# Optimization experiments

Measured on AMD Instinct MI355X. Metric: run time of the kernel, lower is better.

## Reference

```python
import jax, jax.numpy as jnp
import numpy as np

N, E = 10000, 160000
B, F, P, C = 16, 2, 12, 32


def gcn_norm(edge_index, edge_weight, n):
    # GCN symmetric normalization with self-loops (fill value 1.0, improved=False)
    src, dst = edge_index[0], edge_index[1]
    loop = jnp.arange(n, dtype=src.dtype)
    src = jnp.concatenate([src, loop])
    dst = jnp.concatenate([dst, loop])
    w = jnp.concatenate([edge_weight, jnp.ones((n,), edge_weight.dtype)])
    deg = jnp.zeros((n,), w.dtype).at[dst].add(w)
    dinv = jnp.where(deg > 0, jax.lax.rsqrt(deg), 0.0)
    return src, dst, dinv[src] * w * dinv[dst]


def gcn_conv(x, W, b, src, dst, norm, n):
    # x: [B, N, Fin] -> [B, N, Fout]; transform-then-propagate like GCNConv
    xw = x @ W
    msgs = xw[:, src, :] * norm[None, :, None]  # gather over source nodes
    out = jnp.zeros((x.shape[0], n, W.shape[1]), x.dtype).at[:, dst].add(msgs)
    return out + b


def setup_inputs():
    key = jax.random.key(0)
    ks = jax.random.split(key, 20)
    s = 0.1
    return {
        "x": jax.random.normal(ks[0], (B, N, F, P), jnp.float32),
        "edge_index": jax.random.randint(ks[1], (2, E), 0, N, jnp.int32),
        "edge_weight": jax.random.uniform(ks[2], (E,), jnp.float32),
        "W_z": jax.random.normal(ks[3], (F, C), jnp.float32) * s,
        "b_z": jnp.zeros((C,), jnp.float32),
        "lin_z_W": jax.random.normal(ks[4], (2 * C, C), jnp.float32) * s,
        "lin_z_b": jnp.zeros((C,), jnp.float32),
        "W_r": jax.random.normal(ks[5], (F, C), jnp.float32) * s,
        "b_r": jnp.zeros((C,), jnp.float32),
        "lin_r_W": jax.random.normal(ks[6], (2 * C, C), jnp.float32) * s,
        "lin_r_b": jnp.zeros((C,), jnp.float32),
        "W_h": jax.random.normal(ks[7], (F, C), jnp.float32) * s,
        "b_h": jnp.zeros((C,), jnp.float32),
        "lin_h_W": jax.random.normal(ks[8], (2 * C, C), jnp.float32) * s,
        "lin_h_b": jnp.zeros((C,), jnp.float32),
        "attention": jax.random.uniform(ks[9], (P,), jnp.float32),
        "lin_out_W": jax.random.normal(ks[10], (C, P), jnp.float32) * s,
        "lin_out_b": jnp.zeros((P,), jnp.float32),
    }


def reference(x, edge_index, edge_weight, W_z, b_z, lin_z_W, lin_z_b, W_r, b_r,
              lin_r_W, lin_r_b, W_h, b_h, lin_h_W, lin_h_b, attention,
              lin_out_W, lin_out_b):
    b, n, f, p = x.shape
    c = W_z.shape[1]
    src, dst, norm = gcn_norm(edge_index, edge_weight, n)
    probs = jax.nn.softmax(attention)  # attention over periods
    H0 = jnp.zeros((b, n, c), x.dtype)  # A3TGCN2 passes H=None each period
    xs = jnp.moveaxis(x, 3, 0)  # [P, B, N, F]

    def step(acc, inp):
        xp, w = inp  # xp: [B, N, F]
        Gz = gcn_conv(xp, W_z, b_z, src, dst, norm, n)
        Z = jax.nn.sigmoid(jnp.concatenate([Gz, H0], -1) @ lin_z_W + lin_z_b)
        Gr = gcn_conv(xp, W_r, b_r, src, dst, norm, n)
        R = jax.nn.sigmoid(jnp.concatenate([Gr, H0], -1) @ lin_r_W + lin_r_b)
        Gh = gcn_conv(xp, W_h, b_h, src, dst, norm, n)
        Ht = jnp.tanh(jnp.concatenate([Gh, H0 * R], -1) @ lin_h_W + lin_h_b)
        Hn = Z * H0 + (1.0 - Z) * Ht  # one GRU step from zero hidden
        return acc + w * Hn, None

    H_acc, _ = jax.lax.scan(step, H0, (xs, probs))
    h = jax.nn.relu(H_acc)
    return h @ lin_out_W + lin_out_b  # [B, N, periods]
```

## Files before the change

### kernel.cpp

```cpp
#include <hip/hip_runtime.h>
#include <hip/hip_bf16.h>

#define NN 10000
#define EE 160000
#define BB 16
#define PP 12
#define CC 32
#define CAP 64
#define NCB 313
#define NHB 625

__device__ __forceinline__ float fast_rcp(float x){ return __builtin_amdgcn_rcpf(x); }
__device__ __forceinline__ float fast_exp2(float x){
#if __has_builtin(__builtin_amdgcn_exp2f)
    return __builtin_amdgcn_exp2f(x);
#else
    return exp2f(x);
#endif
}
__device__ __forceinline__ unsigned short f2bfu(float f){
    union { float f; unsigned int i; } c; c.f = f;
    unsigned int r = c.i + 0x7FFFu + ((c.i >> 16) & 1u);
    return (unsigned short)(r >> 16);
}
__device__ __forceinline__ void up2(unsigned int u, float& a, float& b){
    union { unsigned int i; float f; } c;
    c.i = u << 16;          a = c.f;
    c.i = u & 0xFFFF0000u;  b = c.f;
}
__device__ __forceinline__ void unp24(uint4 q0, uint4 q1, uint4 q2, float* f){
    up2(q0.x,f[0],f[1]);   up2(q0.y,f[2],f[3]);   up2(q0.z,f[4],f[5]);   up2(q0.w,f[6],f[7]);
    up2(q1.x,f[8],f[9]);   up2(q1.y,f[10],f[11]); up2(q1.z,f[12],f[13]); up2(q1.w,f[14],f[15]);
    up2(q2.x,f[16],f[17]); up2(q2.y,f[18],f[19]); up2(q2.z,f[20],f[21]); up2(q2.w,f[22],f[23]);
}

__global__ __launch_bounds__(256) void k_stage(const float* __restrict__ x,
        const int* __restrict__ srcI, const int* __restrict__ dstI,
        const float* __restrict__ ew,
        unsigned short* __restrict__ xc, float* __restrict__ deg, int* __restrict__ cnt,
        int2* __restrict__ bucket, const int* __restrict__ canary_p,
        const float* __restrict__ Wz, const float* __restrict__ bz,
        const float* __restrict__ LzW, const float* __restrict__ lzb,
        const float* __restrict__ Wh, const float* __restrict__ bh,
        const float* __restrict__ LhW, const float* __restrict__ lhb,
        const float* __restrict__ att, const float* __restrict__ LoW,
        const float* __restrict__ lob, float* __restrict__ wbuf){
    __shared__ unsigned short tile[32*384];
    int bid = blockIdx.x, tid = threadIdx.x;
    if (bid < NCB){
        int n0 = bid*32;
        int n1 = NN - n0; if (n1 > 32) n1 = 32;
        int tot = 16 * n1 * 6;
        for (int i = tid; i < tot; i += 256){
            int b = i / (n1*6);
            int r = i - b*(n1*6);
            float4 f = *(const float4*)(x + b*(NN*24) + n0*24 + r*4);
            ushort4 v; v.x=f2bfu(f.x); v.y=f2bfu(f.y); v.z=f2bfu(f.z); v.w=f2bfu(f.w);
            int nl = (r*4) / 24;
            int fp = (r*4) - nl*24;
            ((ushort4*)tile)[nl*96 + (b*24 + fp)/4] = v;
        }
        __syncthreads();
        int tot4 = n1*48;
        uint4* dst4 = (uint4*)(xc + n0*384);
        for (int i = tid; i < tot4; i += 256)
            dst4[i] = ((const uint4*)tile)[i];
    } else if (bid < NCB + NHB){
        int canary = *canary_p;
        int e = (bid - NCB)*256 + tid;
        int d = dstI[e];
        float w = ew[e];
        atomicAdd(&deg[d], w);
        int rk = atomicAdd(&cnt[d], 1) - canary;
        bucket[d*CAP + rk] = make_int2(srcI[e], __float_as_int(w));
    } else {
        const float L2E = 1.4426950408889634f;
        int c = tid;
        if (c < CC){
            float s0=0.f,s1=0.f,sb=lzb[c], h0=0.f,h1=0.f,hb=lhb[c];
            for (int k=0;k<CC;k++){
                float wz = LzW[k*CC+c];
                s0 += Wz[k]*wz; s1 += Wz[CC+k]*wz; sb += bz[k]*wz;
                float wh = LhW[k*CC+c];
                h0 += Wh[k]*wh; h1 += Wh[CC+k]*wh; hb += bh[k]*wh;
            }
            float* wp = wbuf + c*8;
            wp[0]=s0*L2E; wp[1]=s1*L2E; wp[2]=sb*L2E;
            wp[3]=h0*(2.f*L2E); wp[4]=h1*(2.f*L2E); wp[5]=hb*(2.f*L2E);
            wp[6]=0.f; wp[7]=0.f;
            for (int q=0;q<PP;q++) wbuf[288 + c*PP + q] = LoW[c*PP+q];
        } else if (c == 32){
            float a[PP]; float m = -1e30f;
            for (int p=0;p<PP;p++){ a[p]=att[p]; m = fmaxf(m, a[p]); }
            float s=0.f;
            for (int p=0;p<PP;p++){ a[p]=__expf(a[p]-m); s += a[p]; }
            float r = 1.f/s;
            for (int p=0;p<PP;p++) wbuf[256+p] = a[p]*r;
        } else if (c == 33){
            for (int q=0;q<PP;q++) wbuf[268+q] = lob[q];
        }
    }
}

__global__ __launch_bounds__(256, 4) void k_fused(const unsigned short* __restrict__ xc,
        const int2* __restrict__ bucket, const int* __restrict__ cnt,
        const float* __restrict__ deg, const float* __restrict__ wbuf,
        const int* __restrict__ canary_p, float* __restrict__ out){
    int tid = threadIdx.x;
    int lane = tid & 63;
    int wv   = tid >> 6;
    int h    = lane >> 4;
    int l    = lane & 15;
    int n    = blockIdx.x*4 + wv;
    const unsigned short* xl = xc + l*24;

    int len = cnt[n] - *canary_p;
    float dd = rsqrtf(deg[n] + 1.0f);
    const int2* bp = bucket + n*CAP;

    float acc[24];
    #pragma unroll
    for (int k=0;k<24;k++) acc[k] = 0.f;

    int e = h;
    for (; e + 4 < len; e += 8){
        int2 c1 = bp[e], c2 = bp[e+4];
        float v1 = rsqrtf(deg[c1.x]+1.0f) * __int_as_float(c1.y) * dd;
        float v2 = rsqrtf(deg[c2.x]+1.0f) * __int_as_float(c2.y) * dd;
        const uint4* p1 = (const uint4*)(xl + c1.x*384);
        const uint4* p2 = (const uint4*)(xl + c2.x*384);
        uint4 qa0=p1[0], qa1=p1[1], qa2=p1[2];
        uint4 qb0=p2[0], qb1=p2[1], qb2=p2[2];
        float fa[24], fb[24];
        unp24(qa0,qa1,qa2,fa);
        unp24(qb0,qb1,qb2,fb);
        #pragma unroll
        for (int k=0;k<24;k++) acc[k] = fmaf(v1, fa[k], fmaf(v2, fb[k], acc[k]));
    }
    if (e < len){
        int2 c1 = bp[e];
        float v1 = rsqrtf(deg[c1.x]+1.0f) * __int_as_float(c1.y) * dd;
        const uint4* p1 = (const uint4*)(xl + c1.x*384);
        uint4 qa0=p1[0], qa1=p1[1], qa2=p1[2];
        float fa[24];
        unp24(qa0,qa1,qa2,fa);
        #pragma unroll
        for (int k=0;k<24;k++) acc[k] = fmaf(v1, fa[k], acc[k]);
    }
    if (h == 0){
        float v = dd*dd;
        const uint4* p1 = (const uint4*)(xl + n*384);
        uint4 qa0=p1[0], qa1=p1[1], qa2=p1[2];
        float fa[24];
        unp24(qa0,qa1,qa2,fa);
        #pragma unroll
        for (int k=0;k<24;k++) acc[k] = fmaf(v, fa[k], acc[k]);
    }
    #pragma unroll
    for (int k=0;k<24;k++) acc[k] += __shfl_xor(acc[k], 16, 64);
    #pragma unroll
    for (int k=0;k<24;k++) acc[k] += __shfl_xor(acc[k], 32, 64);

    float pr[12];
    #pragma unroll
    for (int p=0;p<12;p++) pr[p] = wbuf[256+p];
    float o[12];
    #pragma unroll
    for (int q=0;q<12;q++) o[q] = 0.f;
    const float4* wp = (const float4*)wbuf;
    int cbase = h*8;
    #pragma unroll
    for (int cc=0; cc<8; ++cc){
        int c = cbase + cc;
        float4 wa = wp[c*2];
        float4 wb = wp[c*2+1];
        float a = 0.f;
        #pragma unroll
        for (int p=0;p<12;p++){
            float y0 = acc[p], y1 = acc[12+p];
            float zs = fmaf(y1, wa.y, fmaf(y0, wa.x, wa.z));
            float hs = fmaf(y1, wb.x, fmaf(y0, wa.w, wb.y));
            hs = fminf(hs, 80.f);
            float ez = fast_exp2(zs);
            float eh = fast_exp2(hs);
            float den = fmaf(ez, eh, ez) + (eh + 1.f);
            float t  = fast_rcp(den);
            a = fmaf(pr[p]*(eh-1.f), t, a);
        }
        a = fmaxf(a, 0.f);
        const float4* lw = (const float4*)(wbuf + 288 + c*12);
        float4 w0 = lw[0], w1 = lw[1], w2 = lw[2];
        o[0]=fmaf(a,w0.x,o[0]); o[1]=fmaf(a,w0.y,o[1]); o[2] =fmaf(a,w0.z,o[2]);  o[3] =fmaf(a,w0.w,o[3]);
        o[4]=fmaf(a,w1.x,o[4]); o[5]=fmaf(a,w1.y,o[5]); o[6] =fmaf(a,w1.z,o[6]);  o[7] =fmaf(a,w1.w,o[7]);
        o[8]=fmaf(a,w2.x,o[8]); o[9]=fmaf(a,w2.y,o[9]); o[10]=fmaf(a,w2.z,o[10]); o[11]=fmaf(a,w2.w,o[11]);
    }
    #pragma unroll
    for (int q=0;q<12;q++) o[q] += __shfl_xor(o[q], 16, 64);
    #pragma unroll
    for (int q=0;q<12;q++) o[q] += __shfl_xor(o[q], 32, 64);
    if (h == 0){
        #pragma unroll
        for (int q=0;q<12;q++) o[q] += wbuf[268+q];
        float4* op = (float4*)(out + (l*NN + n)*12);
        op[0] = make_float4(o[0],o[1],o[2],o[3]);
        op[1] = make_float4(o[4],o[5],o[6],o[7]);
        op[2] = make_float4(o[8],o[9],o[10],o[11]);
    }
}

extern "C" void kernel_launch(void* const* d_in, const int* in_sizes, int n_in,
                              void* d_out, int out_size, void* d_ws, size_t ws_size,
                              hipStream_t stream) {
    const float* x   = (const float*)d_in[0];
    const int*   ei  = (const int*)d_in[1];
    const float* ew  = (const float*)d_in[2];
    const float* Wz  = (const float*)d_in[3];
    const float* bz  = (const float*)d_in[4];
    const float* LzW = (const float*)d_in[5];
    const float* lzb = (const float*)d_in[6];
    const float* Wh  = (const float*)d_in[11];
    const float* bh  = (const float*)d_in[12];
    const float* LhW = (const float*)d_in[13];
    const float* lhb = (const float*)d_in[14];
    const float* att = (const float*)d_in[15];
    const float* LoW = (const float*)d_in[16];
    const float* lob = (const float*)d_in[17];
    float* out = (float*)d_out;

    const int* srcI = ei;
    const int* dstI = ei + EE;

    char* ws = (char*)d_ws;
    size_t off = 0;
    auto alloc = [&](size_t bytes){ void* p = ws + off; off += (bytes + 255)/256*256; return p; };
    int*            canary = (int*)alloc(256);
    float*          deg    = (float*)alloc((size_t)NN*4);
    int*            cnt    = (int*)alloc((size_t)NN*4);
    float*          wbuf   = (float*)alloc(672*4);
    unsigned short* xc     = (unsigned short*)alloc((size_t)BB*NN*24*2);
    int2*           bucket = (int2*)alloc((size_t)NN*CAP*8);

    hipLaunchKernelGGL(k_stage, dim3(NCB + NHB + 1), dim3(256), 0, stream,
                       x, srcI, dstI, ew, xc, deg, cnt, bucket, canary,
                       Wz, bz, LzW, lzb, Wh, bh, LhW, lhb, att, LoW, lob, wbuf);
    hipLaunchKernelGGL(k_fused, dim3(NN/4), dim3(256), 0, stream,
                       xc, bucket, cnt, deg, wbuf, canary, out);
}
```

Before: 161.2 us.

## Preload edge list per wave and shuffle-broadcast, fold self-loop into loop

The fused kernel now loads each node's whole bucket (up to 64 edges) with one coalesced per-lane load, precomputes the normalized edge weights once per lane, and broadcasts column and weight to the four edge groups with shuffles. The self-loop is folded into the main loop as a virtual edge and the tail branch is removed, at the cost of zero-weight padding gathers on the last iteration. Output stores are split across three lane groups, one float4 each. The staging transpose tile is padded from 384 to 400 elements per node row to reduce LDS bank conflicts.

After: 158.1 us. About the same (-1.9%).

```diff
diff --git a/kernel.cpp b/kernel.cpp
--- a/kernel.cpp
+++ b/kernel.cpp
@@ -45,7 +45,7 @@
         const float* __restrict__ LhW, const float* __restrict__ lhb,
         const float* __restrict__ att, const float* __restrict__ LoW,
         const float* __restrict__ lob, float* __restrict__ wbuf){
-    __shared__ unsigned short tile[32*384];
+    __shared__ unsigned short tile[32*400];
     int bid = blockIdx.x, tid = threadIdx.x;
     if (bid < NCB){
         int n0 = bid*32;
@@ -58,13 +58,16 @@
             ushort4 v; v.x=f2bfu(f.x); v.y=f2bfu(f.y); v.z=f2bfu(f.z); v.w=f2bfu(f.w);
             int nl = (r*4) / 24;
             int fp = (r*4) - nl*24;
-            ((ushort4*)tile)[nl*96 + (b*24 + fp)/4] = v;
+            ((ushort4*)tile)[nl*100 + (b*24 + fp)/4] = v;
         }
         __syncthreads();
         int tot4 = n1*48;
+        const uint4* t4 = (const uint4*)tile;
         uint4* dst4 = (uint4*)(xc + n0*384);
-        for (int i = tid; i < tot4; i += 256)
-            dst4[i] = ((const uint4*)tile)[i];
+        for (int i = tid; i < tot4; i += 256){
+            int nl = i/48, j = i - nl*48;
+            dst4[i] = t4[nl*50 + j];
+        }
     } else if (bid < NCB + NHB){
         int canary = *canary_p;
         int e = (bid - NCB)*256 + tid;
@@ -116,19 +119,26 @@
 
     int len = cnt[n] - *canary_p;
     float dd = rsqrtf(deg[n] + 1.0f);
-    const int2* bp = bucket + n*CAP;
+
+    int2 be = bucket[n*CAP + lane];
+    int   ecol = (lane < len) ? be.x : n;
+    float ewv  = (lane < len) ? __int_as_float(be.y)
+               : (lane == len ? 1.0f : 0.0f);
+    float ev   = rsqrtf(deg[ecol] + 1.0f) * ewv * dd;
 
     float acc[24];
     #pragma unroll
     for (int k=0;k<24;k++) acc[k] = 0.f;
 
-    int e = h;
-    for (; e + 4 < len; e += 8){
-        int2 c1 = bp[e], c2 = bp[e+4];
-        float v1 = rsqrtf(deg[c1.x]+1.0f) * __int_as_float(c1.y) * dd;
-        float v2 = rsqrtf(deg[c2.x]+1.0f) * __int_as_float(c2.y) * dd;
-        const uint4* p1 = (const uint4*)(xl + c1.x*384);
-        const uint4* p2 = (const uint4*)(xl + c2.x*384);
+    int lim = len + 1;
+    for (int eb = 0; eb < lim; eb += 8){
+        int e1 = eb + h, e2 = eb + h + 4;
+        int   c1 = __shfl(ecol, e1, 64);
+        float v1 = __shfl(ev,   e1, 64);
+        int   c2 = __shfl(ecol, e2, 64);
+        float v2 = __shfl(ev,   e2, 64);
+        const uint4* p1 = (const uint4*)(xl + c1*384);
+        const uint4* p2 = (const uint4*)(xl + c2*384);
         uint4 qa0=p1[0], qa1=p1[1], qa2=p1[2];
         uint4 qb0=p2[0], qb1=p2[1], qb2=p2[2];
         float fa[24], fb[24];
@@ -136,25 +146,6 @@
         unp24(qb0,qb1,qb2,fb);
         #pragma unroll
         for (int k=0;k<24;k++) acc[k] = fmaf(v1, fa[k], fmaf(v2, fb[k], acc[k]));
-    }
-    if (e < len){
-        int2 c1 = bp[e];
-        float v1 = rsqrtf(deg[c1.x]+1.0f) * __int_as_float(c1.y) * dd;
-        const uint4* p1 = (const uint4*)(xl + c1.x*384);
-        uint4 qa0=p1[0], qa1=p1[1], qa2=p1[2];
-        float fa[24];
-        unp24(qa0,qa1,qa2,fa);
-        #pragma unroll
-        for (int k=0;k<24;k++) acc[k] = fmaf(v1, fa[k], acc[k]);
-    }
-    if (h == 0){
-        float v = dd*dd;
-        const uint4* p1 = (const uint4*)(xl + n*384);
-        uint4 qa0=p1[0], qa1=p1[1], qa2=p1[2];
-        float fa[24];
-        unp24(qa0,qa1,qa2,fa);
-        #pragma unroll
-        for (int k=0;k<24;k++) acc[k] = fmaf(v, fa[k], acc[k]);
     }
     #pragma unroll
     for (int k=0;k<24;k++) acc[k] += __shfl_xor(acc[k], 16, 64);
@@ -198,13 +189,11 @@
     for (int q=0;q<12;q++) o[q] += __shfl_xor(o[q], 16, 64);
     #pragma unroll
     for (int q=0;q<12;q++) o[q] += __shfl_xor(o[q], 32, 64);
-    if (h == 0){
-        #pragma unroll
-        for (int q=0;q<12;q++) o[q] += wbuf[268+q];
+    #pragma unroll
+    for (int q=0;q<12;q++) o[q] += wbuf[268+q];
+    if (h < 3){
         float4* op = (float4*)(out + (l*NN + n)*12);
-        op[0] = make_float4(o[0],o[1],o[2],o[3]);
-        op[1] = make_float4(o[4],o[5],o[6],o[7]);
-        op[2] = make_float4(o[8],o[9],o[10],o[11]);
+        op[h] = make_float4(o[h*4], o[h*4+1], o[h*4+2], o[h*4+3]);
     }
 }
 
```
